# Kernel tuning notes

Measured on AMD Instinct MI355X. Metric: run time of the kernel, lower is better.

## Reference

```python
import jax, jax.numpy as jnp
import numpy as np

B, S, D = 4, 2048, 1024
EPS = 1e-6


def setup_inputs() -> dict:
    key = jax.random.key(0)
    ks = jax.random.split(key, 9)
    s = 1.0 / np.sqrt(D)
    return {
        "context": jax.random.normal(ks[0], (B, S, D), jnp.float32),
        "eos_mask": jax.random.randint(ks[1], (B, S, S), 0, 2, dtype=jnp.int32),
        "prior": jax.random.uniform(ks[2], (B, S, S), jnp.float32),
        "Wq": jax.random.uniform(ks[3], (D, D), jnp.float32, -s, s),
        "bq": jax.random.uniform(ks[4], (D,), jnp.float32, -s, s),
        "Wk": jax.random.uniform(ks[5], (D, D), jnp.float32, -s, s),
        "bk": jax.random.uniform(ks[6], (D,), jnp.float32, -s, s),
        "gamma": jnp.ones((D,), jnp.float32),
        "beta": jnp.zeros((D,), jnp.float32),
    }


def reference(context, eos_mask, prior, Wq, bq, Wk, bk, gamma, beta):
    d = context.shape[-1]
    seq = context.shape[1]

    # LayerNorm with torch's unbiased std (Bessel correction)
    mean = jnp.mean(context, axis=-1, keepdims=True)
    var = jnp.sum((context - mean) ** 2, axis=-1, keepdims=True) / (d - 1)
    x = gamma * (context - mean) / (jnp.sqrt(var) + EPS) + beta

    q = x @ Wq + bq  # linear_query
    k = x @ Wk + bk  # linear_key

    scores = jnp.einsum("bid,bjd->bij", q, k) / d  # note: /d, not /sqrt(d)

    idx = jnp.arange(seq)
    band = jnp.abs(idx[:, None] - idx[None, :]) == 1      # a + c (tridiagonal off-diagonals)
    sup = (idx[None, :] - idx[:, None]) == 1              # a (superdiagonal)
    strict_upper = idx[:, None] < idx[None, :]            # triu(ones) - eye
    eye = idx[:, None] == idx[None, :]

    mask = (eos_mask != 0) & band[None]                   # eos_mask & (a + c)
    scores = jnp.where(mask, scores, -1e9)
    na = jax.nn.softmax(scores, axis=-1)
    na = jnp.sqrt(na * jnp.swapaxes(na, -1, -2) + 1e-9)
    na = prior + (1.0 - prior) * na                       # hier_add_index branch

    # t = log(na+eps).masked_fill(a==0,0) @ triu  ==  cumsum along last axis
    t = jnp.where(sup[None], jnp.log(na + 1e-9), 0.0)
    t = jnp.cumsum(t, axis=-1)
    # g = triu @ t  ==  reversed cumsum along axis -2
    g = jnp.cumsum(t[..., ::-1, :], axis=-2)[..., ::-1, :]
    g = jnp.where(strict_upper[None], jnp.exp(g), 0.0)

    g_attn = g + jnp.swapaxes(g, -1, -2) + jnp.where(eye[None], na, 1e-9)
    return (g_attn, na)
```

## Files before the change

### kernel.cpp

```cpp
#include <hip/hip_runtime.h>
#include <hip/hip_bf16.h>
#include <cmath>

#define BB 4
#define SS 2048
#define DD 1024
#define BS (BB*SS)
constexpr float EPS = 1e-6f;

typedef __attribute__((ext_vector_type(8))) short short8;
typedef __attribute__((ext_vector_type(4))) float floatx4;

__device__ inline float bf2f(unsigned short u) {
    unsigned v = ((unsigned)u) << 16;
    float f; __builtin_memcpy(&f, &v, 4);
    return f;
}

__global__ __launch_bounds__(256)
void prep_kernel(const float* __restrict__ Wq, const float* __restrict__ Wk,
                 const float* __restrict__ bq, const float* __restrict__ bk,
                 __hip_bfloat16* __restrict__ Wb, float* __restrict__ u,
                 float* __restrict__ v, float* __restrict__ cs,
                 float* __restrict__ sacc) {
    int blk = blockIdx.x;
    if (blk < 2048) {
        int idx = blk * 256 + threadIdx.x;
        const int half = DD * DD / 4;
        const float* src = (idx < half) ? Wk : Wq;
        int off = (idx < half) ? idx : idx - half;
        float4 val = ((const float4*)src)[off];
        union { ushort4 uu; __hip_bfloat16 h[4]; } pk;
        pk.h[0] = __float2bfloat16(val.x);
        pk.h[1] = __float2bfloat16(val.y);
        pk.h[2] = __float2bfloat16(val.z);
        pk.h[3] = __float2bfloat16(val.w);
        ((ushort4*)Wb)[idx] = pk.uu;
    } else if (blk < 2561) {
        int gid = (blk - 2048) * 4 + (threadIdx.x >> 6);
        int lane = threadIdx.x & 63;
        if (gid > 2048) return;
        const float* row; const float* vec; float* outp;
        if (gid < 1024)      { row = Wq + (size_t)gid * DD;          vec = bk; outp = u + gid; }
        else if (gid < 2048) { row = Wk + (size_t)(gid - 1024) * DD; vec = bq; outp = v + (gid - 1024); }
        else                 { row = bq;                             vec = bk; outp = cs; }
        float s = 0.f;
        #pragma unroll
        for (int k = 0; k < 4; ++k) {
            float4 a = ((const float4*)row)[lane * 4 + k];
            float4 b = ((const float4*)vec)[lane * 4 + k];
            s += a.x * b.x + a.y * b.y + a.z * b.z + a.w * b.w;
        }
        #pragma unroll
        for (int off = 32; off; off >>= 1) s += __shfl_down(s, off);
        if (lane == 0) *outp = s;
    } else {
        int idx = (blk - 2561) * 1024 + threadIdx.x * 4;
        *(float4*)(sacc + idx) = make_float4(0.f, 0.f, 0.f, 0.f);
    }
}

__global__ __launch_bounds__(256)
void ln_kernel(const float* __restrict__ ctx, const float* __restrict__ gamma,
               const float* __restrict__ beta, const float* __restrict__ u,
               const float* __restrict__ v, const float* __restrict__ cs,
               __hip_bfloat16* __restrict__ xo, float* __restrict__ alpha,
               float* __restrict__ betav) {
    int row = blockIdx.x;
    int t = threadIdx.x;
    const float* r = ctx + (size_t)row * DD;
    float4 val = ((const float4*)r)[t];
    float s1 = val.x + val.y + val.z + val.w;
    float s2 = val.x*val.x + val.y*val.y + val.z*val.z + val.w*val.w;
    #pragma unroll
    for (int off = 32; off; off >>= 1) {
        s1 += __shfl_down(s1, off);
        s2 += __shfl_down(s2, off);
    }
    __shared__ float ls1[4], ls2[4];
    int wid = t >> 6, lane = t & 63;
    if (lane == 0) { ls1[wid] = s1; ls2[wid] = s2; }
    __syncthreads();
    if (t == 0) {
        float a = ls1[0] + ls1[1] + ls1[2] + ls1[3];
        float b = ls2[0] + ls2[1] + ls2[2] + ls2[3];
        float mean = a / DD;
        float var = (b - a * a / DD) / (DD - 1);
        ls1[0] = mean;
        ls2[0] = 1.0f / (sqrtf(var) + EPS);
    }
    __syncthreads();
    float mean = ls1[0], rstd = ls2[0];
    float4 g = ((const float4*)gamma)[t];
    float4 be = ((const float4*)beta)[t];
    float nx0 = g.x * (val.x - mean) * rstd + be.x;
    float nx1 = g.y * (val.y - mean) * rstd + be.y;
    float nx2 = g.z * (val.z - mean) * rstd + be.z;
    float nx3 = g.w * (val.w - mean) * rstd + be.w;
    union { ushort4 uu; __hip_bfloat16 h[4]; } pk;
    pk.h[0] = __float2bfloat16(nx0);
    pk.h[1] = __float2bfloat16(nx1);
    pk.h[2] = __float2bfloat16(nx2);
    pk.h[3] = __float2bfloat16(nx3);
    ((ushort4*)(xo + (size_t)row * DD))[t] = pk.uu;
    float4 u4 = ((const float4*)u)[t];
    float4 v4 = ((const float4*)v)[t];
    float du = nx0 * u4.x + nx1 * u4.y + nx2 * u4.z + nx3 * u4.w;
    float dv = nx0 * v4.x + nx1 * v4.y + nx2 * v4.z + nx3 * v4.w;
    #pragma unroll
    for (int off = 32; off; off >>= 1) {
        du += __shfl_down(du, off);
        dv += __shfl_down(dv, off);
    }
    __syncthreads();
    if (lane == 0) { ls1[wid] = du; ls2[wid] = dv; }
    __syncthreads();
    if (t == 0) {
        alpha[row] = ls1[0] + ls1[1] + ls1[2] + ls1[3] + *cs;
        betav[row] = ls2[0] + ls2[1] + ls2[2] + ls2[3];
    }
}

__global__ __launch_bounds__(256)
void gemm64_mfma(const __hip_bfloat16* __restrict__ A,
                 const __hip_bfloat16* __restrict__ B,
                 __hip_bfloat16* __restrict__ C, int ldc) {
    __shared__ short As[64 * 64];
    __shared__ short Bs[64 * 64];
    int tid = threadIdx.x;
    int wave = tid >> 6;
    int lane = tid & 63;
    int q = lane >> 4, m16 = lane & 15;
    int srow = lane >> 3;
    int skoff = (lane & 7) * 8;

    const __hip_bfloat16* gA = A + ((size_t)blockIdx.x * 64 + wave * 16 + srow) * DD + skoff;
    const __hip_bfloat16* gB = B + ((size_t)blockIdx.y * 64 + wave * 16 + srow) * DD + skoff;
    short* lA0 = As + (wave * 16) * 64;
    short* lA1 = As + (wave * 16 + 8) * 64;
    short* lB0 = Bs + (wave * 16) * 64;
    short* lB1 = Bs + (wave * 16 + 8) * 64;

    floatx4 acc[4] = {};
    for (int k0 = 0; k0 < DD; k0 += 64) {
        __builtin_amdgcn_global_load_lds(
            (const __attribute__((address_space(1))) void*)(gA + k0),
            (__attribute__((address_space(3))) void*)(lA0), 16, 0, 0);
        __builtin_amdgcn_global_load_lds(
            (const __attribute__((address_space(1))) void*)(gA + k0 + 8 * DD),
            (__attribute__((address_space(3))) void*)(lA1), 16, 0, 0);
        __builtin_amdgcn_global_load_lds(
            (const __attribute__((address_space(1))) void*)(gB + k0),
            (__attribute__((address_space(3))) void*)(lB0), 16, 0, 0);
        __builtin_amdgcn_global_load_lds(
            (const __attribute__((address_space(1))) void*)(gB + k0 + 8 * DD),
            (__attribute__((address_space(3))) void*)(lB1), 16, 0, 0);
        __syncthreads();
        #pragma unroll
        for (int h = 0; h < 2; ++h) {
            short8 af = *(const short8*)(As + (wave * 16 + m16) * 64 + h * 32 + q * 8);
            #pragma unroll
            for (int c = 0; c < 4; ++c) {
                short8 bf_ = *(const short8*)(Bs + (c * 16 + m16) * 64 + h * 32 + q * 8);
                acc[c] = __builtin_amdgcn_mfma_f32_16x16x32_bf16(af, bf_, acc[c], 0, 0, 0);
            }
        }
        __syncthreads();
    }
    #pragma unroll
    for (int c = 0; c < 4; ++c) {
        int gcol = blockIdx.y * 64 + c * 16 + m16;
        #pragma unroll
        for (int e = 0; e < 4; ++e) {
            int grow = blockIdx.x * 64 + wave * 16 + q * 4 + e;
            C[(size_t)grow * ldc + gcol] = __float2bfloat16(acc[c][e]);
        }
    }
}

#define TM 128
#define TN 128
#define TK 32
__global__ __launch_bounds__(256)
void gemm2_fused(const __hip_bfloat16* __restrict__ A,
                 const __hip_bfloat16* __restrict__ B,
                 float* __restrict__ sacc) {
    __shared__ short smem[18432];
    short* As = smem;
    short* Bs = smem + TM * TK;
    int tid = threadIdx.x;
    int wave = tid >> 6;
    int lane = tid & 63;
    int wm = wave >> 1, wn = wave & 1;
    int q = lane >> 4, m16 = lane & 15;

    int srow = lane >> 2;
    int skoff = (lane & 3) * 8;
    const __hip_bfloat16* gA = A + ((size_t)blockIdx.x * TM + wave * 32 + srow) * DD + skoff;
    const __hip_bfloat16* gB = B + ((size_t)blockIdx.y * TN + wave * 32 + srow) * DD + skoff;
    short* lAbase = As + (wave * 32) * TK;
    short* lBbase = Bs + (wave * 32) * TK;

    floatx4 acc[4][4] = {};

    for (int k0 = 0; k0 < DD; k0 += TK) {
        __builtin_amdgcn_global_load_lds(
            (const __attribute__((address_space(1))) void*)(gA + k0),
            (__attribute__((address_space(3))) void*)(lAbase), 16, 0, 0);
        __builtin_amdgcn_global_load_lds(
            (const __attribute__((address_space(1))) void*)(gA + k0 + 16 * DD),
            (__attribute__((address_space(3))) void*)(lAbase + 16 * TK), 16, 0, 0);
        __builtin_amdgcn_global_load_lds(
            (const __attribute__((address_space(1))) void*)(gB + k0),
            (__attribute__((address_space(3))) void*)(lBbase), 16, 0, 0);
        __builtin_amdgcn_global_load_lds(
            (const __attribute__((address_space(1))) void*)(gB + k0 + 16 * DD),
            (__attribute__((address_space(3))) void*)(lBbase + 16 * TK), 16, 0, 0);
        __syncthreads();
        short8 af[4], bf_[4];
        #pragma unroll
        for (int r = 0; r < 4; ++r)
            af[r] = *(const short8*)(As + (wm * 64 + r * 16 + m16) * TK + q * 8);
        #pragma unroll
        for (int c = 0; c < 4; ++c)
            bf_[c] = *(const short8*)(Bs + (wn * 64 + c * 16 + m16) * TK + q * 8);
        #pragma unroll
        for (int r = 0; r < 4; ++r)
            #pragma unroll
            for (int c = 0; c < 4; ++c)
                acc[r][c] = __builtin_amdgcn_mfma_f32_16x16x32_bf16(af[r], bf_[c], acc[r][c], 0, 0, 0);
        __syncthreads();
    }

    short* EP = smem + wave * 4608;
    #pragma unroll
    for (int r = 0; r < 4; ++r)
        #pragma unroll
        for (int c = 0; c < 4; ++c)
            #pragma unroll
            for (int e = 0; e < 4; ++e) {
                __hip_bfloat16 hv = __float2bfloat16(acc[r][c][e]);
                EP[(r * 16 + q * 4 + e) * 72 + c * 16 + m16] = *(short*)&hv;
            }

    int rl = lane;
    int growZ = blockIdx.x * TM + wm * 64 + rl;
    int gcol0 = blockIdx.y * TN + wn * 64;
    float zf[64];
    #pragma unroll
    for (int c8 = 0; c8 < 8; ++c8) {
        short8 zz = *(const short8*)(EP + rl * 72 + c8 * 8);
        #pragma unroll
        for (int e = 0; e < 8; ++e) zf[c8 * 8 + e] = bf2f((unsigned short)zz[e]);
    }
    if (growZ + 1 < BS) {
        const short8* px = (const short8*)(A + (size_t)(growZ + 1) * DD + gcol0);
        float sup = 0.f;
        #pragma unroll
        for (int c8 = 0; c8 < 8; ++c8) {
            short8 xx = px[c8];
            #pragma unroll
            for (int e = 0; e < 8; ++e) sup += zf[c8 * 8 + e] * bf2f((unsigned short)xx[e]);
        }
        atomicAdd(&sacc[growZ], sup);
    }
    if (growZ >= 1) {
        const short8* px = (const short8*)(A + (size_t)(growZ - 1) * DD + gcol0);
        float sub = 0.f;
        #pragma unroll
        for (int c8 = 0; c8 < 8; ++c8) {
            short8 xx = px[c8];
            #pragma unroll
            for (int e = 0; e < 8; ++e) sub += zf[c8 * 8 + e] * bf2f((unsigned short)xx[e]);
        }
        atomicAdd(&sacc[BS + growZ], sub);
    }
}

__global__ __launch_bounds__(256)
void softmax_kernel(const float* __restrict__ sacc, const int* __restrict__ eos,
                    const float* __restrict__ alpha, const float* __restrict__ betav,
                    float* __restrict__ vsub, float* __restrict__ vsup,
                    float* __restrict__ wuni) {
    int gw = blockIdx.x * 256 + threadIdx.x;
    int i = gw & (SS - 1);
    float a = alpha[gw];
    float ssup = 0.f, ssub = 0.f;
    if (i < SS - 1) ssup = (sacc[gw] + a + betav[gw + 1]) * (1.0f / DD);
    if (i > 0)      ssub = (sacc[BS + gw] + a + betav[gw - 1]) * (1.0f / DD);
    bool msub = (i > 0) && (eos[(size_t)gw * SS + (i - 1)] != 0);
    bool msup = (i < SS - 1) && (eos[(size_t)gw * SS + (i + 1)] != 0);
    float vs, vp, w;
    if (msub && msup) {
        float mx = fmaxf(ssub, ssup);
        float e1 = expf(ssub - mx), e2 = expf(ssup - mx);
        float inv = 1.0f / (e1 + e2);
        vs = e1 * inv; vp = e2 * inv; w = 0.f;
    } else if (msub) { vs = 1.f; vp = 0.f; w = 0.f; }
    else if (msup)   { vs = 0.f; vp = 1.f; w = 0.f; }
    else             { vs = vp = w = 1.0f / SS; }
    vsub[gw] = vs; vsup[gw] = vp; wuni[gw] = w;
}

__global__ __launch_bounds__(256)
void scan_kernel(const float* __restrict__ prior, const float* __restrict__ vsub,
                 const float* __restrict__ vsup, double* __restrict__ Lc) {
    int b = blockIdx.x;
    int t = threadIdx.x;
    double loc[8];
    double s = 0.0;
    #pragma unroll
    for (int k = 0; k < 8; ++k) {
        int tt = t * 8 + k;
        double Lv = 0.0;
        if (tt < SS - 1) {
            float pr = prior[((size_t)(b * SS + tt)) * SS + tt + 1];
            float na2 = sqrtf(vsup[b * SS + tt] * vsub[b * SS + tt + 1] + 1e-9f);
            float P = pr + (1.f - pr) * na2;
            Lv = log((double)P + 1e-9);
        }
        loc[k] = Lv; s += Lv;
    }
    __shared__ double sa[256], sb[256];
    sa[t] = s;
    __syncthreads();
    double* src = sa; double* dst = sb;
    for (int off = 1; off < 256; off <<= 1) {
        double v = src[t];
        if (t >= off) v += src[t - off];
        __syncthreads();
        dst[t] = v;
        __syncthreads();
        double* tmp = src; src = dst; dst = tmp;
    }
    double run = (t == 0) ? 0.0 : src[t - 1];
    #pragma unroll
    for (int k = 0; k < 8; ++k) {
        int idx = t * 8 + k;
        Lc[b * SS + idx] = run;
        run += loc[k];
    }
}

__global__ __launch_bounds__(256)
void out_kernel(const float* __restrict__ prior, const float* __restrict__ vsub,
                const float* __restrict__ vsup, const float* __restrict__ wuni,
                const double* __restrict__ Lc, float* __restrict__ out_g,
                float* __restrict__ out_na) {
    size_t gid = (size_t)blockIdx.x * 256 + threadIdx.x;
    int jt = (int)(gid & 511);
    int row = (int)(gid >> 9);
    int i = row & (SS - 1);
    int b = row >> 11;
    int j0 = jt * 4;
    size_t base = (size_t)row * SS + j0;
    float4 pr4 = *(const float4*)(prior + base);
    float4 wj4 = *(const float4*)(wuni + b * SS + j0);
    float pra[4] = {pr4.x, pr4.y, pr4.z, pr4.w};
    float wja[4] = {wj4.x, wj4.y, wj4.z, wj4.w};
    float wi = wuni[row];
    double Lci = Lc[row];
    const double* Lcb = Lc + b * SS;
    float nav[4], gv[4];
    #pragma unroll
    for (int c = 0; c < 4; ++c) {
        int j = j0 + c;
        float prod;
        if (j == i - 1)      prod = vsub[row] * vsup[row - 1];
        else if (j == i + 1) prod = vsup[row] * vsub[row + 1];
        else if (j == i)     prod = wi * wi;
        else                 prod = wi * wja[c];
        float na2 = sqrtf(prod + 1e-9f);
        float p = pra[c];
        float na3 = p + (1.f - p) * na2;
        nav[c] = na3;
        if (j == i) {
            gv[c] = na3;
        } else {
            double d = (j > i) ? (Lcb[j] - Lci) : (Lci - Lcb[j]);
            gv[c] = expf((float)d) + 1e-9f;
        }
    }
    *(float4*)(out_g + base) = make_float4(gv[0], gv[1], gv[2], gv[3]);
    *(float4*)(out_na + base) = make_float4(nav[0], nav[1], nav[2], nav[3]);
}

extern "C" void kernel_launch(void* const* d_in, const int* in_sizes, int n_in,
                              void* d_out, int out_size, void* d_ws, size_t ws_size,
                              hipStream_t stream) {
    const float* ctx   = (const float*)d_in[0];
    const int*   eos   = (const int*)d_in[1];
    const float* prior = (const float*)d_in[2];
    const float* Wq    = (const float*)d_in[3];
    const float* bq    = (const float*)d_in[4];
    const float* Wk    = (const float*)d_in[5];
    const float* bk    = (const float*)d_in[6];
    const float* gamma = (const float*)d_in[7];
    const float* beta  = (const float*)d_in[8];

    float* out_g  = (float*)d_out;
    float* out_na = out_g + (size_t)BB * SS * SS;

    char* ws = (char*)d_ws;
    size_t o = 0;
    __hip_bfloat16* x  = (__hip_bfloat16*)(ws + o); o += (size_t)BS * DD * 2;
    __hip_bfloat16* Wb = (__hip_bfloat16*)(ws + o); o += (size_t)2 * DD * DD * 2;
    __hip_bfloat16* Mt = (__hip_bfloat16*)(ws + o); o += (size_t)DD * DD * 2;
    double* Lc   = (double*)(ws + o); o += (size_t)BS * 8;
    float* u     = (float*)(ws + o);  o += DD * 4;
    float* v     = (float*)(ws + o);  o += DD * 4;
    float* cs    = (float*)(ws + o);  o += 64;
    float* alpha = (float*)(ws + o);  o += (size_t)BS * 4;
    float* betav = (float*)(ws + o);  o += (size_t)BS * 4;
    float* vsub  = (float*)(ws + o);  o += (size_t)BS * 4;
    float* vsup  = (float*)(ws + o);  o += (size_t)BS * 4;
    float* wuni  = (float*)(ws + o);  o += (size_t)BS * 4;
    float* sacc  = (float*)(ws + o);  o += (size_t)2 * BS * 4;

    __hip_bfloat16* Wk_bf = Wb;
    __hip_bfloat16* Wq_bf = Wb + (size_t)DD * DD;

    prep_kernel<<<2577, 256, 0, stream>>>(Wq, Wk, bq, bk, Wb, u, v, cs, sacc);
    ln_kernel<<<BS, 256, 0, stream>>>(ctx, gamma, beta, u, v, cs, x, alpha, betav);

    dim3 g1(DD / 64, DD / 64);
    gemm64_mfma<<<g1, 256, 0, stream>>>(Wk_bf, Wq_bf, Mt, DD);

    dim3 g2(BS / TM, DD / TN);
    gemm2_fused<<<g2, 256, 0, stream>>>(x, Mt, sacc);

    softmax_kernel<<<BS / 256, 256, 0, stream>>>(sacc, eos, alpha, betav, vsub, vsup, wuni);

    scan_kernel<<<BB, 256, 0, stream>>>(prior, vsub, vsup, Lc);

    size_t total = (size_t)BB * SS * SS / 4;
    out_kernel<<<(int)(total / 256), 256, 0, stream>>>(prior, vsub, vsup, wuni, Lc,
                                                       out_g, out_na);
}
```

Before: 326.7 us.

## Fuse weight conversion into Mt GEMM, drop atomics, merge softmax with scan

The separate fp32-to-bf16 weight conversion pass is removed. The Wk·Wq^T GEMM now loads fp32 weights, converts them in registers and writes padded LDS tiles, and the u/v/cs GEMVs run in the same launch. The two atomicAdd reductions in the second GEMM's epilogue become plain stores into 16 per-row partial slots, so the zeroing pass is no longer needed. The softmax kernel is merged into the scan kernel, which sums those slots and keeps vsub/vsup in shared memory. The trade-off is that the softmax work now runs on only 4 blocks instead of 32, and the 16-slot buffers add extra memory traffic.

```diff
diff --git a/kernel.cpp b/kernel.cpp
--- a/kernel.cpp
+++ b/kernel.cpp
@@ -16,29 +16,24 @@
     float f; __builtin_memcpy(&f, &v, 4);
     return f;
 }
+__device__ inline short f2bf_s(float f) {
+    __hip_bfloat16 h = __float2bfloat16(f);
+    short s; __builtin_memcpy(&s, &h, 2);
+    return s;
+}
 
 __global__ __launch_bounds__(256)
-void prep_kernel(const float* __restrict__ Wq, const float* __restrict__ Wk,
-                 const float* __restrict__ bq, const float* __restrict__ bk,
-                 __hip_bfloat16* __restrict__ Wb, float* __restrict__ u,
-                 float* __restrict__ v, float* __restrict__ cs,
-                 float* __restrict__ sacc) {
+void mtgemv_kernel(const float* __restrict__ Wq, const float* __restrict__ Wk,
+                   const float* __restrict__ bq, const float* __restrict__ bk,
+                   __hip_bfloat16* __restrict__ Mt, float* __restrict__ u,
+                   float* __restrict__ v, float* __restrict__ cs) {
+    __shared__ short As[64 * 72];
+    __shared__ short Bs[64 * 72];
     int blk = blockIdx.x;
-    if (blk < 2048) {
-        int idx = blk * 256 + threadIdx.x;
-        const int half = DD * DD / 4;
-        const float* src = (idx < half) ? Wk : Wq;
-        int off = (idx < half) ? idx : idx - half;
-        float4 val = ((const float4*)src)[off];
-        union { ushort4 uu; __hip_bfloat16 h[4]; } pk;
-        pk.h[0] = __float2bfloat16(val.x);
-        pk.h[1] = __float2bfloat16(val.y);
-        pk.h[2] = __float2bfloat16(val.z);
-        pk.h[3] = __float2bfloat16(val.w);
-        ((ushort4*)Wb)[idx] = pk.uu;
-    } else if (blk < 2561) {
-        int gid = (blk - 2048) * 4 + (threadIdx.x >> 6);
-        int lane = threadIdx.x & 63;
+    int tid = threadIdx.x;
+    if (blk >= 256) {
+        int gid = (blk - 256) * 4 + (tid >> 6);
+        int lane = tid & 63;
         if (gid > 2048) return;
         const float* row; const float* vec; float* outp;
         if (gid < 1024)      { row = Wq + (size_t)gid * DD;          vec = bk; outp = u + gid; }
@@ -54,9 +49,60 @@
         #pragma unroll
         for (int off = 32; off; off >>= 1) s += __shfl_down(s, off);
         if (lane == 0) *outp = s;
-    } else {
-        int idx = (blk - 2561) * 1024 + threadIdx.x * 4;
-        *(float4*)(sacc + idx) = make_float4(0.f, 0.f, 0.f, 0.f);
+        return;
+    }
+    int bx = blk & 15, by = blk >> 4;
+    int wave = tid >> 6;
+    int lane = tid & 63;
+    int q = lane >> 4, m16 = lane & 15;
+    int sr = tid >> 2;
+    int skc = (tid & 3) * 16;
+
+    const float* gA = Wk + (size_t)(bx * 64 + sr) * DD + skc;
+    const float* gB = Wq + (size_t)(by * 64 + sr) * DD + skc;
+
+    floatx4 acc[4] = {};
+    for (int k0 = 0; k0 < DD; k0 += 64) {
+        {
+            const float4* p = (const float4*)(gA + k0);
+            float4 a0 = p[0], a1 = p[1], a2 = p[2], a3 = p[3];
+            short8 s0 = { f2bf_s(a0.x), f2bf_s(a0.y), f2bf_s(a0.z), f2bf_s(a0.w),
+                          f2bf_s(a1.x), f2bf_s(a1.y), f2bf_s(a1.z), f2bf_s(a1.w) };
+            short8 s1 = { f2bf_s(a2.x), f2bf_s(a2.y), f2bf_s(a2.z), f2bf_s(a2.w),
+                          f2bf_s(a3.x), f2bf_s(a3.y), f2bf_s(a3.z), f2bf_s(a3.w) };
+            *(short8*)(As + sr * 72 + skc) = s0;
+            *(short8*)(As + sr * 72 + skc + 8) = s1;
+        }
+        {
+            const float4* p = (const float4*)(gB + k0);
+            float4 a0 = p[0], a1 = p[1], a2 = p[2], a3 = p[3];
+            short8 s0 = { f2bf_s(a0.x), f2bf_s(a0.y), f2bf_s(a0.z), f2bf_s(a0.w),
+                          f2bf_s(a1.x), f2bf_s(a1.y), f2bf_s(a1.z), f2bf_s(a1.w) };
+            short8 s1 = { f2bf_s(a2.x), f2bf_s(a2.y), f2bf_s(a2.z), f2bf_s(a2.w),
+                          f2bf_s(a3.x), f2bf_s(a3.y), f2bf_s(a3.z), f2bf_s(a3.w) };
+            *(short8*)(Bs + sr * 72 + skc) = s0;
+            *(short8*)(Bs + sr * 72 + skc + 8) = s1;
+        }
+        __syncthreads();
+        #pragma unroll
+        for (int h = 0; h < 2; ++h) {
+            short8 af = *(const short8*)(As + (wave * 16 + m16) * 72 + h * 32 + q * 8);
+            #pragma unroll
+            for (int c = 0; c < 4; ++c) {
+                short8 bf_ = *(const short8*)(Bs + (c * 16 + m16) * 72 + h * 32 + q * 8);
+                acc[c] = __builtin_amdgcn_mfma_f32_16x16x32_bf16(af, bf_, acc[c], 0, 0, 0);
+            }
+        }
+        __syncthreads();
+    }
+    #pragma unroll
+    for (int c = 0; c < 4; ++c) {
+        int gcol = by * 64 + c * 16 + m16;
+        #pragma unroll
+        for (int e = 0; e < 4; ++e) {
+            int grow = bx * 64 + wave * 16 + q * 4 + e;
+            Mt[(size_t)grow * DD + gcol] = __float2bfloat16(acc[c][e]);
+        }
     }
 }
 
@@ -121,70 +167,13 @@
     }
 }
 
-__global__ __launch_bounds__(256)
-void gemm64_mfma(const __hip_bfloat16* __restrict__ A,
-                 const __hip_bfloat16* __restrict__ B,
-                 __hip_bfloat16* __restrict__ C, int ldc) {
-    __shared__ short As[64 * 64];
-    __shared__ short Bs[64 * 64];
-    int tid = threadIdx.x;
-    int wave = tid >> 6;
-    int lane = tid & 63;
-    int q = lane >> 4, m16 = lane & 15;
-    int srow = lane >> 3;
-    int skoff = (lane & 7) * 8;
-
-    const __hip_bfloat16* gA = A + ((size_t)blockIdx.x * 64 + wave * 16 + srow) * DD + skoff;
-    const __hip_bfloat16* gB = B + ((size_t)blockIdx.y * 64 + wave * 16 + srow) * DD + skoff;
-    short* lA0 = As + (wave * 16) * 64;
-    short* lA1 = As + (wave * 16 + 8) * 64;
-    short* lB0 = Bs + (wave * 16) * 64;
-    short* lB1 = Bs + (wave * 16 + 8) * 64;
-
-    floatx4 acc[4] = {};
-    for (int k0 = 0; k0 < DD; k0 += 64) {
-        __builtin_amdgcn_global_load_lds(
-            (const __attribute__((address_space(1))) void*)(gA + k0),
-            (__attribute__((address_space(3))) void*)(lA0), 16, 0, 0);
-        __builtin_amdgcn_global_load_lds(
-            (const __attribute__((address_space(1))) void*)(gA + k0 + 8 * DD),
-            (__attribute__((address_space(3))) void*)(lA1), 16, 0, 0);
-        __builtin_amdgcn_global_load_lds(
-            (const __attribute__((address_space(1))) void*)(gB + k0),
-            (__attribute__((address_space(3))) void*)(lB0), 16, 0, 0);
-        __builtin_amdgcn_global_load_lds(
-            (const __attribute__((address_space(1))) void*)(gB + k0 + 8 * DD),
-            (__attribute__((address_space(3))) void*)(lB1), 16, 0, 0);
-        __syncthreads();
-        #pragma unroll
-        for (int h = 0; h < 2; ++h) {
-            short8 af = *(const short8*)(As + (wave * 16 + m16) * 64 + h * 32 + q * 8);
-            #pragma unroll
-            for (int c = 0; c < 4; ++c) {
-                short8 bf_ = *(const short8*)(Bs + (c * 16 + m16) * 64 + h * 32 + q * 8);
-                acc[c] = __builtin_amdgcn_mfma_f32_16x16x32_bf16(af, bf_, acc[c], 0, 0, 0);
-            }
-        }
-        __syncthreads();
-    }
-    #pragma unroll
-    for (int c = 0; c < 4; ++c) {
-        int gcol = blockIdx.y * 64 + c * 16 + m16;
-        #pragma unroll
-        for (int e = 0; e < 4; ++e) {
-            int grow = blockIdx.x * 64 + wave * 16 + q * 4 + e;
-            C[(size_t)grow * ldc + gcol] = __float2bfloat16(acc[c][e]);
-        }
-    }
-}
-
 #define TM 128
 #define TN 128
 #define TK 32
 __global__ __launch_bounds__(256)
 void gemm2_fused(const __hip_bfloat16* __restrict__ A,
                  const __hip_bfloat16* __restrict__ B,
-                 float* __restrict__ sacc) {
+                 float* __restrict__ sacc, float* __restrict__ sacc2) {
     __shared__ short smem[18432];
     short* As = smem;
     short* Bs = smem + TM * TK;
@@ -238,14 +227,13 @@
         #pragma unroll
         for (int c = 0; c < 4; ++c)
             #pragma unroll
-            for (int e = 0; e < 4; ++e) {
-                __hip_bfloat16 hv = __float2bfloat16(acc[r][c][e]);
-                EP[(r * 16 + q * 4 + e) * 72 + c * 16 + m16] = *(short*)&hv;
-            }
+            for (int e = 0; e < 4; ++e)
+                EP[(r * 16 + q * 4 + e) * 72 + c * 16 + m16] = f2bf_s(acc[r][c][e]);
 
     int rl = lane;
     int growZ = blockIdx.x * TM + wm * 64 + rl;
     int gcol0 = blockIdx.y * TN + wn * 64;
+    int slot = blockIdx.y * 2 + wn;
     float zf[64];
     #pragma unroll
     for (int c8 = 0; c8 < 8; ++c8) {
@@ -262,7 +250,7 @@
             #pragma unroll
             for (int e = 0; e < 8; ++e) sup += zf[c8 * 8 + e] * bf2f((unsigned short)xx[e]);
         }
-        atomicAdd(&sacc[growZ], sup);
+        sacc[(size_t)growZ * 16 + slot] = sup;
     }
     if (growZ >= 1) {
         const short8* px = (const short8*)(A + (size_t)(growZ - 1) * DD + gcol0);
@@ -273,40 +261,54 @@
             #pragma unroll
             for (int e = 0; e < 8; ++e) sub += zf[c8 * 8 + e] * bf2f((unsigned short)xx[e]);
         }
-        atomicAdd(&sacc[BS + growZ], sub);
+        sacc2[(size_t)growZ * 16 + slot] = sub;
     }
 }
 
 __global__ __launch_bounds__(256)
-void softmax_kernel(const float* __restrict__ sacc, const int* __restrict__ eos,
-                    const float* __restrict__ alpha, const float* __restrict__ betav,
-                    float* __restrict__ vsub, float* __restrict__ vsup,
-                    float* __restrict__ wuni) {
-    int gw = blockIdx.x * 256 + threadIdx.x;
-    int i = gw & (SS - 1);
-    float a = alpha[gw];
-    float ssup = 0.f, ssub = 0.f;
-    if (i < SS - 1) ssup = (sacc[gw] + a + betav[gw + 1]) * (1.0f / DD);
-    if (i > 0)      ssub = (sacc[BS + gw] + a + betav[gw - 1]) * (1.0f / DD);
-    bool msub = (i > 0) && (eos[(size_t)gw * SS + (i - 1)] != 0);
-    bool msup = (i < SS - 1) && (eos[(size_t)gw * SS + (i + 1)] != 0);
-    float vs, vp, w;
-    if (msub && msup) {
-        float mx = fmaxf(ssub, ssup);
-        float e1 = expf(ssub - mx), e2 = expf(ssup - mx);
-        float inv = 1.0f / (e1 + e2);
-        vs = e1 * inv; vp = e2 * inv; w = 0.f;
-    } else if (msub) { vs = 1.f; vp = 0.f; w = 0.f; }
-    else if (msup)   { vs = 0.f; vp = 1.f; w = 0.f; }
-    else             { vs = vp = w = 1.0f / SS; }
-    vsub[gw] = vs; vsup[gw] = vp; wuni[gw] = w;
-}
-
-__global__ __launch_bounds__(256)
-void scan_kernel(const float* __restrict__ prior, const float* __restrict__ vsub,
-                 const float* __restrict__ vsup, double* __restrict__ Lc) {
+void softscan_kernel(const float* __restrict__ sacc, const float* __restrict__ sacc2,
+                     const int* __restrict__ eos, const float* __restrict__ alpha,
+                     const float* __restrict__ betav, const float* __restrict__ prior,
+                     float* __restrict__ vsub, float* __restrict__ vsup,
+                     float* __restrict__ wuni, double* __restrict__ Lc) {
     int b = blockIdx.x;
     int t = threadIdx.x;
+    __shared__ float vs_s[SS];
+    __shared__ float vp_s[SS];
+    #pragma unroll
+    for (int k = 0; k < 8; ++k) {
+        int i = t * 8 + k;
+        int gw = b * SS + i;
+        float ssup = 0.f, ssub = 0.f;
+        if (i < SS - 1) {
+            const float4* p = (const float4*)(sacc + (size_t)gw * 16);
+            float4 a0 = p[0], a1 = p[1], a2 = p[2], a3 = p[3];
+            float s = a0.x + a0.y + a0.z + a0.w + a1.x + a1.y + a1.z + a1.w
+                    + a2.x + a2.y + a2.z + a2.w + a3.x + a3.y + a3.z + a3.w;
+            ssup = (s + alpha[gw] + betav[gw + 1]) * (1.0f / DD);
+        }
+        if (i > 0) {
+            const float4* p = (const float4*)(sacc2 + (size_t)gw * 16);
+            float4 a0 = p[0], a1 = p[1], a2 = p[2], a3 = p[3];
+            float s = a0.x + a0.y + a0.z + a0.w + a1.x + a1.y + a1.z + a1.w
+                    + a2.x + a2.y + a2.z + a2.w + a3.x + a3.y + a3.z + a3.w;
+            ssub = (s + alpha[gw] + betav[gw - 1]) * (1.0f / DD);
+        }
+        bool msub = (i > 0) && (eos[(size_t)gw * SS + (i - 1)] != 0);
+        bool msup = (i < SS - 1) && (eos[(size_t)gw * SS + (i + 1)] != 0);
+        float vs, vp, w;
+        if (msub && msup) {
+            float mx = fmaxf(ssub, ssup);
+            float e1 = expf(ssub - mx), e2 = expf(ssup - mx);
+            float inv = 1.0f / (e1 + e2);
+            vs = e1 * inv; vp = e2 * inv; w = 0.f;
+        } else if (msub) { vs = 1.f; vp = 0.f; w = 0.f; }
+        else if (msup)   { vs = 0.f; vp = 1.f; w = 0.f; }
+        else             { vs = vp = w = 1.0f / SS; }
+        vs_s[i] = vs; vp_s[i] = vp;
+        vsub[gw] = vs; vsup[gw] = vp; wuni[gw] = w;
+    }
+    __syncthreads();
     double loc[8];
     double s = 0.0;
     #pragma unroll
@@ -315,7 +317,7 @@
         double Lv = 0.0;
         if (tt < SS - 1) {
             float pr = prior[((size_t)(b * SS + tt)) * SS + tt + 1];
-            float na2 = sqrtf(vsup[b * SS + tt] * vsub[b * SS + tt + 1] + 1e-9f);
+            float na2 = sqrtf(vp_s[tt] * vs_s[tt + 1] + 1e-9f);
             float P = pr + (1.f - pr) * na2;
             Lv = log((double)P + 1e-9);
         }
@@ -404,7 +406,6 @@
     char* ws = (char*)d_ws;
     size_t o = 0;
     __hip_bfloat16* x  = (__hip_bfloat16*)(ws + o); o += (size_t)BS * DD * 2;
-    __hip_bfloat16* Wb = (__hip_bfloat16*)(ws + o); o += (size_t)2 * DD * DD * 2;
     __hip_bfloat16* Mt = (__hip_bfloat16*)(ws + o); o += (size_t)DD * DD * 2;
     double* Lc   = (double*)(ws + o); o += (size_t)BS * 8;
     float* u     = (float*)(ws + o);  o += DD * 4;
@@ -415,23 +416,18 @@
     float* vsub  = (float*)(ws + o);  o += (size_t)BS * 4;
     float* vsup  = (float*)(ws + o);  o += (size_t)BS * 4;
     float* wuni  = (float*)(ws + o);  o += (size_t)BS * 4;
-    float* sacc  = (float*)(ws + o);  o += (size_t)2 * BS * 4;
-
-    __hip_bfloat16* Wk_bf = Wb;
-    __hip_bfloat16* Wq_bf = Wb + (size_t)DD * DD;
-
-    prep_kernel<<<2577, 256, 0, stream>>>(Wq, Wk, bq, bk, Wb, u, v, cs, sacc);
+    float* sacc  = (float*)(ws + o);  o += (size_t)BS * 16 * 4;
+    float* sacc2 = (float*)(ws + o);  o += (size_t)BS * 16 * 4;
+
+    mtgemv_kernel<<<769, 256, 0, stream>>>(Wq, Wk, bq, bk, Mt, u, v, cs);
+
     ln_kernel<<<BS, 256, 0, stream>>>(ctx, gamma, beta, u, v, cs, x, alpha, betav);
 
-    dim3 g1(DD / 64, DD / 64);
-    gemm64_mfma<<<g1, 256, 0, stream>>>(Wk_bf, Wq_bf, Mt, DD);
-
     dim3 g2(BS / TM, DD / TN);
-    gemm2_fused<<<g2, 256, 0, stream>>>(x, Mt, sacc);
-
-    softmax_kernel<<<BS / 256, 256, 0, stream>>>(sacc, eos, alpha, betav, vsub, vsup, wuni);
-
-    scan_kernel<<<BB, 256, 0, stream>>>(prior, vsub, vsup, Lc);
+    gemm2_fused<<<g2, 256, 0, stream>>>(x, Mt, sacc, sacc2);
+
+    softscan_kernel<<<BB, 256, 0, stream>>>(sacc, sacc2, eos, alpha, betav, prior,
+                                            vsub, vsup, wuni, Lc);
 
     size_t total = (size_t)BB * SS * SS / 4;
     out_kernel<<<(int)(total / 256), 256, 0, stream>>>(prior, vsub, vsup, wuni, Lc,
```

Measured after the change: 342.0 us. 1.05x slower.
